# Kernel tuning notes

Hardware: AMD Instinct MI355X
Metric: run time of the kernel (lower is better)

The kernel has to match this reference:

```python
import jax, jax.numpy as jnp
import numpy as np

BETA = 0.25  # commitment_beta


def setup_inputs() -> dict:
    key = jax.random.key(0)
    k1, k2 = jax.random.split(key)
    B, S, D, K = 4, 2048, 256, 8192
    z_e = jax.random.normal(k1, (B, S, D), dtype=jnp.float32)
    # codebook init ~ uniform(-1/K, 1/K) in the original; scale is irrelevant for correctness,
    # use normal scaled similarly small.
    codebook = jax.random.uniform(k2, (K, D), dtype=jnp.float32, minval=-1.0 / K, maxval=1.0 / K)
    return {"z_e": z_e, "codebook": codebook}


def reference(z_e, codebook):
    B, S, D = z_e.shape
    flat = z_e.reshape(-1, D)  # [N, D], N = B*S
    distances = (
        jnp.sum(flat * flat, axis=1, keepdims=True)
        - 2.0 * (flat @ codebook.T)
        + jnp.sum(codebook * codebook, axis=1)[None, :]
    )
    indices = jnp.argmin(distances, axis=1)  # [N]
    z_q = codebook[indices].reshape(B, S, D)
    codebook_loss = jnp.mean((jax.lax.stop_gradient(z_e) - z_q) ** 2)
    commitment_loss = jnp.mean((z_e - jax.lax.stop_gradient(z_q)) ** 2)
    vq_loss = codebook_loss + BETA * commitment_loss
    # straight-through estimator
    z_q_st = z_e + jax.lax.stop_gradient(z_q - z_e)
    return z_q_st, indices.reshape(B, S), vq_loss
```

## Files before the change

kernel.cpp:

```cpp
#include <hip/hip_runtime.h>
#include <stdint.h>

#define N_ROWS  8192
#define DIM     256
#define K_CODES 8192
#define SPLITK  16
#define KS      512
#define NT      128
#define LSLOTS  15
#define GSLOTS  8
#define MARGIN_ACC 1.0e-4f
#define MARGIN_FIN 2.5e-4f

typedef unsigned long long u64;
typedef unsigned short u16;
typedef short s16x8 __attribute__((ext_vector_type(8)));
typedef float f32x4 __attribute__((ext_vector_type(4)));

__device__ __forceinline__ u64 u64min(u64 a, u64 b) { return a < b ? a : b; }

__device__ __forceinline__ u16 f2bf(float f) {
    unsigned u = __float_as_uint(f);
    u += 0x7fffu + ((u >> 16) & 1u);
    return (u16)(u >> 16);
}

__device__ __forceinline__ void gld16(void* lds, const void* g) {
    __builtin_amdgcn_global_load_lds(
        (const __attribute__((address_space(1))) unsigned int*)g,
        (__attribute__((address_space(3))) unsigned int*)lds, 16, 0, 0);
}

__device__ __forceinline__ void block_barrier() {
    asm volatile("" ::: "memory");
    __builtin_amdgcn_s_barrier();
    asm volatile("" ::: "memory");
}

__global__ __launch_bounds__(256) void vq_prep(const float* __restrict__ z_e,
                                               const float* __restrict__ cb,
                                               u16* __restrict__ zb,
                                               u16* __restrict__ cbb,
                                               float* __restrict__ xnorm,
                                               float* __restrict__ cnorm) {
    int wid  = (blockIdx.x * 256 + threadIdx.x) >> 6;
    int lane = threadIdx.x & 63;
    const float* src; u16* d16; float* dn;
    if (wid < N_ROWS) { src = z_e + (size_t)wid * DIM; d16 = zb + (size_t)wid * DIM; dn = xnorm + wid; }
    else              { int k = wid - N_ROWS;
                        src = cb  + (size_t)k   * DIM; d16 = cbb + (size_t)k * DIM; dn = cnorm + k; }
    float4 v = *(const float4*)(src + lane * 4);
    ushort4 h;
    h.x = f2bf(v.x); h.y = f2bf(v.y); h.z = f2bf(v.z); h.w = f2bf(v.w);
    *(ushort4*)(d16 + lane * 4) = h;
    float s = (v.x * v.x + v.y * v.y) + (v.z * v.z + v.w * v.w);
#pragma unroll
    for (int off = 1; off < 64; off <<= 1)
        s += __shfl_xor(s, off, 64);
    if (lane == 0) *dn = s;
}

__global__ __launch_bounds__(256, 2) void vq_mfma(const u16* __restrict__ zb,
                                                  const u16* __restrict__ cbb,
                                                  int* __restrict__ cand_cnt,
                                                  unsigned* __restrict__ cand_pk) {
    __shared__ u16   Cs[2][128 * 64];
    __shared__ float lcd[128 * LSLOTS];
    __shared__ int   lci[128 * LSLOTS];
    __shared__ int   lcnt[128];
    __shared__ float gmaxs[128];

    const int tid   = threadIdx.x;
    const int lane  = tid & 63;
    const int wave  = tid >> 6;
    const int quad  = lane >> 4;
    const int l16   = lane & 15;
    const int split = blockIdx.x;
    const int n0    = blockIdx.y * 128;

    if (tid < 128) lcnt[tid] = 0;

    const int srow8  = lane >> 3;
    const int schunk = lane & 7;
    const int ssw    = (schunk ^ srow8) * 8;
    const u16* csrc  = cbb + (size_t)split * KS * DIM + (size_t)srow8 * DIM + ssw;

    s16x8 af[2][8];
#pragma unroll
    for (int i = 0; i < 2; i++) {
        const u16* p = zb + (size_t)(n0 + wave * 32 + i * 16 + l16) * DIM + quad * 8;
#pragma unroll
        for (int s = 0; s < 8; s++)
            af[i][s] = *(const s16x8*)(p + s * 32);
    }

    auto STAGE = [&](int s, int slot) {
        const u16* src = csrc + (size_t)(s >> 2) * (NT * DIM) + (s & 3) * 64;
#pragma unroll
        for (int t = 0; t < 4; t++) {
            int rg = wave * 4 + t;
            gld16(&Cs[slot][rg * 512], src + (size_t)rg * (8 * DIM));
        }
    };

    float runmax[8];
#pragma unroll
    for (int t = 0; t < 8; t++) runmax[t] = -3.0e38f;

    STAGE(0, 0);
    asm volatile("s_waitcnt vmcnt(0) lgkmcnt(0)" ::: "memory");
    block_barrier();

    for (int kt = 0; kt < KS / NT; kt++) {
        const int kbase = split * KS + kt * NT;
        f32x4 acc[2][8];
#pragma unroll
        for (int i = 0; i < 2; i++)
#pragma unroll
            for (int j = 0; j < 8; j++)
#pragma unroll
                for (int e = 0; e < 4; e++) acc[i][j][e] = 0.0f;

#pragma unroll
        for (int kc = 0; kc < 4; kc++) {
            const int it = (kt << 2) | kc;
            if (it < 15) STAGE(it + 1, (it + 1) & 1);

            const u16* cbuf = &Cs[it & 1][0];
#pragma unroll
            for (int ks = 0; ks < 2; ks++) {
                s16x8 bfr[8];
#pragma unroll
                for (int j = 0; j < 8; j++)
                    bfr[j] = *(const s16x8*)&cbuf[(j * 16 + l16) * 64 +
                                                  (((ks << 2) | quad) ^ (l16 & 7)) * 8];
#pragma unroll
                for (int i = 0; i < 2; i++)
#pragma unroll
                    for (int j = 0; j < 8; j++)
                        acc[i][j] = __builtin_amdgcn_mfma_f32_16x16x32_bf16(
                            af[i][kc * 2 + ks], bfr[j], acc[i][j], 0, 0, 0);
            }

            if (it < 15) {
                asm volatile("s_waitcnt vmcnt(0) lgkmcnt(0)" ::: "memory");
                block_barrier();
            }
        }

#pragma unroll
        for (int i = 0; i < 2; i++)
#pragma unroll
            for (int r = 0; r < 4; r++) {
                float m = fmaxf(fmaxf(fmaxf(acc[i][0][r], acc[i][1][r]),
                                      fmaxf(acc[i][2][r], acc[i][3][r])),
                                fmaxf(fmaxf(acc[i][4][r], acc[i][5][r]),
                                      fmaxf(acc[i][6][r], acc[i][7][r])));
                m = fmaxf(m, __shfl_xor(m, 1, 64));
                m = fmaxf(m, __shfl_xor(m, 2, 64));
                m = fmaxf(m, __shfl_xor(m, 4, 64));
                m = fmaxf(m, __shfl_xor(m, 8, 64));
                runmax[i * 4 + r] = fmaxf(runmax[i * 4 + r], m);
                float thr = runmax[i * 4 + r] - MARGIN_ACC;
                int rl = wave * 32 + i * 16 + quad * 4 + r;
#pragma unroll
                for (int j = 0; j < 8; j++) {
                    float d = acc[i][j][r];
                    if (d >= thr) {
                        int pos = atomicAdd(&lcnt[rl], 1);
                        if (pos < LSLOTS) {
                            lcd[rl * LSLOTS + pos] = d;
                            lci[rl * LSLOTS + pos] = kbase + j * 16 + l16;
                        }
                    }
                }
            }
    }

    if (l16 == 0) {
#pragma unroll
        for (int i = 0; i < 2; i++)
#pragma unroll
            for (int r = 0; r < 4; r++)
                gmaxs[wave * 32 + i * 16 + quad * 4 + r] = runmax[i * 4 + r];
    }
    __syncthreads();

    if (tid < 128) {
        int n   = n0 + tid;
        int cnt = lcnt[tid]; if (cnt > LSLOTS) cnt = LSLOTS;
        float thrf = gmaxs[tid] - MARGIN_ACC;
        float bd[GSLOTS]; int bi[GSLOTS];
        int w = 0;
        for (int s = 0; s < cnt; s++) {
            float d = lcd[tid * LSLOTS + s];
            if (d < thrf) continue;
            if (w < GSLOTS) { bd[w] = d; bi[w] = lci[tid * LSLOTS + s]; w++; }
            else {
                int mn = 0;
#pragma unroll
                for (int k = 1; k < GSLOTS; k++) if (bd[k] < bd[mn]) mn = k;
                if (d > bd[mn]) { bd[mn] = d; bi[mn] = lci[tid * LSLOTS + s]; }
            }
        }
        int base = (split * N_ROWS + n) * GSLOTS;
        for (int k = 0; k < w; k++)
            cand_pk[base + k] = ((unsigned)f2bf(bd[k]) << 16) | (unsigned)bi[k];
        cand_cnt[split * N_ROWS + n] = w;
    }
}

__global__ __launch_bounds__(256) void vq_finalize(const float* __restrict__ z_e,
                                                   const float* __restrict__ cb,
                                                   const float* __restrict__ xnorm,
                                                   const float* __restrict__ cnorm,
                                                   const int* __restrict__ cand_cnt,
                                                   const unsigned* __restrict__ cand_pk,
                                                   float* __restrict__ out_zq,
                                                   float* __restrict__ out_idx,
                                                   float* __restrict__ rowloss) {
    const int n    = blockIdx.x * 4 + (threadIdx.x >> 6);
    const int lane = threadIdx.x & 63;

    int   myidx = -1;
    float mydot = -3.0e38f;
    int t = 0;
#pragma unroll
    for (int s = 0; s < SPLITK; s++) {
        int c = cand_cnt[s * N_ROWS + n];
        if (lane >= t && lane < t + c) {
            unsigned key = cand_pk[(s * N_ROWS + n) * GSLOTS + (lane - t)];
            myidx = (int)(key & 0x1FFFu);
            mydot = __uint_as_float(key & 0xFFFF0000u);
        }
        t += c;
    }

    float mg = mydot;
#pragma unroll
    for (int off = 1; off < 64; off <<= 1)
        mg = fmaxf(mg, __shfl_xor(mg, off, 64));

    u64 key = ~0ULL;
    if (myidx >= 0 && mydot >= mg - MARGIN_FIN) {
        const float* xr = z_e + (size_t)n * DIM;
        const float* cr = cb + (size_t)myidx * DIM;
        float acc = 0.0f;
#pragma unroll 8
        for (int d = 0; d < DIM; d++)
            acc = __builtin_fmaf(xr[d], cr[d], acc);
        float dist = __builtin_fmaf(-2.0f, acc, xnorm[n]) + cnorm[myidx];
        key = ((u64)__float_as_uint(dist) << 32) | (unsigned)myidx;
    }
#pragma unroll
    for (int off = 1; off < 64; off <<= 1)
        key = u64min(key, __shfl_xor(key, off, 64));

    int idx = (int)(unsigned)(key & 0xffffffffu);
    if (key == ~0ULL) idx = 0;

    float4 x = *(const float4*)(z_e + (size_t)n * DIM + lane * 4);
    float4 c = *(const float4*)(cb + (size_t)idx * DIM + lane * 4);
    float4 st;
    st.x = x.x + (c.x - x.x); st.y = x.y + (c.y - x.y);
    st.z = x.z + (c.z - x.z); st.w = x.w + (c.w - x.w);
    *(float4*)(out_zq + (size_t)n * DIM + lane * 4) = st;

    float d0 = x.x - c.x, d1 = x.y - c.y, d2 = x.z - c.z, d3 = x.w - c.w;
    float s2 = (d0 * d0 + d1 * d1) + (d2 * d2 + d3 * d3);
#pragma unroll
    for (int off = 1; off < 64; off <<= 1)
        s2 += __shfl_xor(s2, off, 64);
    if (lane == 0) {
        rowloss[n] = s2;
        out_idx[n] = (float)idx;
    }
}

__global__ __launch_bounds__(256) void vq_loss(const float* __restrict__ rowloss,
                                               float* __restrict__ out_loss) {
    __shared__ double sd[256];
    double s = 0.0;
    for (int i = threadIdx.x; i < N_ROWS; i += 256) s += (double)rowloss[i];
    sd[threadIdx.x] = s;
    __syncthreads();
    for (int off = 128; off; off >>= 1) {
        if (threadIdx.x < off) sd[threadIdx.x] += sd[threadIdx.x + off];
        __syncthreads();
    }
    if (threadIdx.x == 0) {
        double mean = sd[0] / (double)((size_t)N_ROWS * DIM);
        out_loss[0] = (float)(1.25 * mean);
    }
}

extern "C" void kernel_launch(void* const* d_in, const int* in_sizes, int n_in,
                              void* d_out, int out_size, void* d_ws, size_t ws_size,
                              hipStream_t stream) {
    const float* z_e = (const float*)d_in[0];
    const float* cb  = (const float*)d_in[1];

    float* out   = (float*)d_out;
    float* zq    = out;
    float* oidx  = out + (size_t)N_ROWS * DIM;
    float* oloss = oidx + N_ROWS;

    u16*      zb       = (u16*)d_ws;
    u16*      cbb      = zb + (size_t)N_ROWS * DIM;
    float*    xnorm    = (float*)(cbb + (size_t)K_CODES * DIM);
    float*    cnorm    = xnorm + N_ROWS;
    float*    rowloss  = cnorm + K_CODES;
    int*      cand_cnt = (int*)(rowloss + N_ROWS);
    unsigned* cand_pk  = (unsigned*)(cand_cnt + N_ROWS * SPLITK);

    vq_prep    <<<(N_ROWS + K_CODES) / 4, 256, 0, stream>>>(z_e, cb, zb, cbb, xnorm, cnorm);
    vq_mfma    <<<dim3(SPLITK, N_ROWS / 128), 256, 0, stream>>>(zb, cbb, cand_cnt, cand_pk);
    vq_finalize<<<N_ROWS / 4, 256, 0, stream>>>(z_e, cb, xnorm, cnorm, cand_cnt, cand_pk,
                                                zq, oidx, rowloss);
    vq_loss    <<<1, 256, 0, stream>>>(rowloss, oloss);
}
```

Before: 185.3 us.

## Give each wave a private codebook LDS ring and drop block barriers

Each wave now stages its own codebook copy into a private double-buffered LDS ring, 32 codes by 64 dims per stage, and waits on its own vmcnt instead of using block-wide barriers. The code tile per epilogue shrinks from 128 to 32 codes, so the accumulator count drops from 16 to 4 fragments per wave. This removes barrier stalls and lowers register pressure. In exchange, every wave loads the full codebook slice separately, which quadruples global/L2 traffic for codebook tiles, and the candidate-selection epilogue with its shuffles runs four times as often.

```diff
diff --git a/kernel.cpp b/kernel.cpp
--- a/kernel.cpp
+++ b/kernel.cpp
@@ -6,7 +6,6 @@
 #define K_CODES 8192
 #define SPLITK  16
 #define KS      512
-#define NT      128
 #define LSLOTS  15
 #define GSLOTS  8
 #define MARGIN_ACC 1.0e-4f
@@ -29,12 +28,6 @@
     __builtin_amdgcn_global_load_lds(
         (const __attribute__((address_space(1))) unsigned int*)g,
         (__attribute__((address_space(3))) unsigned int*)lds, 16, 0, 0);
-}
-
-__device__ __forceinline__ void block_barrier() {
-    asm volatile("" ::: "memory");
-    __builtin_amdgcn_s_barrier();
-    asm volatile("" ::: "memory");
 }
 
 __global__ __launch_bounds__(256) void vq_prep(const float* __restrict__ z_e,
@@ -64,7 +57,7 @@
                                                   const u16* __restrict__ cbb,
                                                   int* __restrict__ cand_cnt,
                                                   unsigned* __restrict__ cand_pk) {
-    __shared__ u16   Cs[2][128 * 64];
+    __shared__ u16   Cs[4][2][32 * 64];
     __shared__ float lcd[128 * LSLOTS];
     __shared__ int   lci[128 * LSLOTS];
     __shared__ int   lcnt[128];
@@ -79,6 +72,7 @@
     const int n0    = blockIdx.y * 128;
 
     if (tid < 128) lcnt[tid] = 0;
+    __syncthreads();
 
     const int srow8  = lane >> 3;
     const int schunk = lane & 7;
@@ -94,57 +88,59 @@
             af[i][s] = *(const s16x8*)(p + s * 32);
     }
 
-    auto STAGE = [&](int s, int slot) {
-        const u16* src = csrc + (size_t)(s >> 2) * (NT * DIM) + (s & 3) * 64;
-#pragma unroll
-        for (int t = 0; t < 4; t++) {
-            int rg = wave * 4 + t;
-            gld16(&Cs[slot][rg * 512], src + (size_t)rg * (8 * DIM));
-        }
+    u16* const ring0 = &Cs[wave][0][0];
+    u16* const ring1 = &Cs[wave][1][0];
+
+    auto STAGE = [&](int s) {
+        const int ct = s >> 2, kc = s & 3;
+        u16* dst = (s & 1) ? ring1 : ring0;
+        const u16* src = csrc + (size_t)(ct * 32) * DIM + kc * 64;
+#pragma unroll
+        for (int t = 0; t < 4; t++)
+            gld16(dst + t * 512, src + (size_t)(t * 8) * DIM);
     };
 
+    f32x4 acc[2][2];
     float runmax[8];
 #pragma unroll
     for (int t = 0; t < 8; t++) runmax[t] = -3.0e38f;
 
-    STAGE(0, 0);
-    asm volatile("s_waitcnt vmcnt(0) lgkmcnt(0)" ::: "memory");
-    block_barrier();
-
-    for (int kt = 0; kt < KS / NT; kt++) {
-        const int kbase = split * KS + kt * NT;
-        f32x4 acc[2][8];
+    STAGE(0);
+
+    for (int ct = 0; ct < 16; ct++) {
+        const int cb0 = split * KS + ct * 32;
 #pragma unroll
         for (int i = 0; i < 2; i++)
 #pragma unroll
-            for (int j = 0; j < 8; j++)
+            for (int j = 0; j < 2; j++)
 #pragma unroll
                 for (int e = 0; e < 4; e++) acc[i][j][e] = 0.0f;
 
 #pragma unroll
         for (int kc = 0; kc < 4; kc++) {
-            const int it = (kt << 2) | kc;
-            if (it < 15) STAGE(it + 1, (it + 1) & 1);
-
-            const u16* cbuf = &Cs[it & 1][0];
+            const int s = ct * 4 + kc;
+            if (s < 63) {
+                asm volatile("s_waitcnt lgkmcnt(0)" ::: "memory");
+                STAGE(s + 1);
+                asm volatile("s_waitcnt vmcnt(4)" ::: "memory");
+            } else {
+                asm volatile("s_waitcnt vmcnt(0)" ::: "memory");
+            }
+
+            const u16* cbuf = (s & 1) ? ring1 : ring0;
 #pragma unroll
             for (int ks = 0; ks < 2; ks++) {
-                s16x8 bfr[8];
-#pragma unroll
-                for (int j = 0; j < 8; j++)
-                    bfr[j] = *(const s16x8*)&cbuf[(j * 16 + l16) * 64 +
-                                                  (((ks << 2) | quad) ^ (l16 & 7)) * 8];
+                s16x8 bfr[2];
+#pragma unroll
+                for (int jj = 0; jj < 2; jj++)
+                    bfr[jj] = *(const s16x8*)&cbuf[(jj * 16 + l16) * 64 +
+                                                   (((ks << 2) | quad) ^ (l16 & 7)) * 8];
 #pragma unroll
                 for (int i = 0; i < 2; i++)
 #pragma unroll
-                    for (int j = 0; j < 8; j++)
-                        acc[i][j] = __builtin_amdgcn_mfma_f32_16x16x32_bf16(
-                            af[i][kc * 2 + ks], bfr[j], acc[i][j], 0, 0, 0);
-            }
-
-            if (it < 15) {
-                asm volatile("s_waitcnt vmcnt(0) lgkmcnt(0)" ::: "memory");
-                block_barrier();
+                    for (int jj = 0; jj < 2; jj++)
+                        acc[i][jj] = __builtin_amdgcn_mfma_f32_16x16x32_bf16(
+                            af[i][kc * 2 + ks], bfr[jj], acc[i][jj], 0, 0, 0);
             }
         }
 
@@ -152,10 +148,7 @@
         for (int i = 0; i < 2; i++)
 #pragma unroll
             for (int r = 0; r < 4; r++) {
-                float m = fmaxf(fmaxf(fmaxf(acc[i][0][r], acc[i][1][r]),
-                                      fmaxf(acc[i][2][r], acc[i][3][r])),
-                                fmaxf(fmaxf(acc[i][4][r], acc[i][5][r]),
-                                      fmaxf(acc[i][6][r], acc[i][7][r])));
+                float m = fmaxf(acc[i][0][r], acc[i][1][r]);
                 m = fmaxf(m, __shfl_xor(m, 1, 64));
                 m = fmaxf(m, __shfl_xor(m, 2, 64));
                 m = fmaxf(m, __shfl_xor(m, 4, 64));
@@ -164,13 +157,13 @@
                 float thr = runmax[i * 4 + r] - MARGIN_ACC;
                 int rl = wave * 32 + i * 16 + quad * 4 + r;
 #pragma unroll
-                for (int j = 0; j < 8; j++) {
-                    float d = acc[i][j][r];
+                for (int jj = 0; jj < 2; jj++) {
+                    float d = acc[i][jj][r];
                     if (d >= thr) {
                         int pos = atomicAdd(&lcnt[rl], 1);
                         if (pos < LSLOTS) {
                             lcd[rl * LSLOTS + pos] = d;
-                            lci[rl * LSLOTS + pos] = kbase + j * 16 + l16;
+                            lci[rl * LSLOTS + pos] = cb0 + jj * 16 + l16;
                         }
                     }
                 }
```

New measurement: 241.0 us. 1.3x slower.
